# Kernel tuning notes

Hardware: AMD Instinct MI355X
Metric: run time of the kernel (lower is better)

Reference implementation:

```python
import jax, jax.numpy as jnp
import numpy as np

N_HEADS = 12
LN_EPS = 1e-5


def _layernorm(x, w):
    # torch F.layer_norm (no affine) then * w
    x = x.astype(jnp.float32)
    mu = jnp.mean(x, axis=-1, keepdims=True)
    var = jnp.mean(jnp.square(x - mu), axis=-1, keepdims=True)
    return (x - mu) * jax.lax.rsqrt(var + LN_EPS) * w


def _rotate_half(x):
    x1, x2 = jnp.split(x, 2, axis=-1)
    return jnp.concatenate([-x2, x1], axis=-1)


def setup_inputs() -> dict:
    key = jax.random.key(0)
    ks = jax.random.split(key, 10)
    b, s, dim, cond, hd = 2, 4096, 768, 768, 64
    mlp = 4 * dim
    # rotary tables
    inv_freq = 1.0 / (10000.0 ** (np.arange(0, hd, 2, dtype=np.float32) / hd))
    t = np.arange(s, dtype=np.float32)
    freqs = np.einsum('s,d->sd', t, inv_freq)           # [s, hd/2]
    emb = np.concatenate([freqs, freqs], axis=-1)        # [s, hd]
    cos = jnp.asarray(np.cos(emb))[None, :, None, None, :]
    sin = jnp.asarray(np.sin(emb))[None, :, None, None, :]
    sc = lambda f: 1.0 / np.sqrt(f)
    return {
        'x': jax.random.normal(ks[0], (b, s, dim), jnp.float32),
        'cos': cos,
        'sin': sin,
        'c': jax.random.normal(ks[1], (b, cond), jnp.float32),
        'attention_mask': jax.random.randint(ks[2], (b, s), 0, 2, jnp.int32),
        'ln1_w': jnp.ones((dim,), jnp.float32),
        'Wqkv': jax.random.normal(ks[3], (3 * dim, dim), jnp.float32) * sc(dim),
        'Wout': jax.random.normal(ks[4], (dim, dim), jnp.float32) * sc(dim),
        'ln2_w': jnp.ones((dim,), jnp.float32),
        'W1': jax.random.normal(ks[5], (mlp, dim), jnp.float32) * sc(dim),
        'b1': jnp.zeros((mlp,), jnp.float32),
        'W2': jax.random.normal(ks[6], (dim, mlp), jnp.float32) * sc(mlp),
        'b2': jnp.zeros((dim,), jnp.float32),
        'Wada': jax.random.normal(ks[7], (6 * dim, cond), jnp.float32) * 0.02,
        'bada': jnp.zeros((6 * dim,), jnp.float32),
    }


def reference(x, cos, sin, c, attention_mask, ln1_w, Wqkv, Wout, ln2_w, W1, b1, W2, b2, Wada, bada):
    b, s, dim = x.shape
    h, hd = N_HEADS, dim // N_HEADS
    # adaLN modulation: [b, 6*dim] -> six [b, 1, dim] chunks
    mod = (c @ Wada.T + bada)[:, None, :]
    shift_msa, scale_msa, gate_msa, shift_mlp, scale_mlp, gate_mlp = jnp.split(mod, 6, axis=2)

    x_skip = x
    hdn = _layernorm(x, ln1_w) * (1.0 + scale_msa) + shift_msa
    qkv = (hdn @ Wqkv.T).reshape(b, s, 3, h, hd)
    qkv = qkv * cos + _rotate_half(qkv) * sin            # RoPE on q, k, and v (as in source)
    q = jnp.transpose(qkv[:, :, 0], (0, 2, 1, 3))        # [b, h, s, hd]
    k = jnp.transpose(qkv[:, :, 1], (0, 2, 1, 3))
    v = jnp.transpose(qkv[:, :, 2], (0, 2, 1, 3))

    m = attention_mask.astype(bool)
    pair = m[:, None, :, None] & m[:, None, None, :]     # [b, 1, s, s]
    bias = jnp.where(pair, 0.0, -1e9).astype(q.dtype)

    scores = jnp.einsum('bhqd,bhkd->bhqk', q, k) / jnp.sqrt(jnp.asarray(hd, q.dtype))
    attn = jax.nn.softmax(scores + bias, axis=-1)
    o = jnp.einsum('bhqk,bhkd->bhqd', attn, v)
    o = jnp.transpose(o, (0, 2, 1, 3)).reshape(b, s, dim)

    # inference-mode bias_dropout_add_scale (dropout off)
    x = x_skip + gate_msa * (o @ Wout.T)
    h2 = _layernorm(x, ln2_w) * (1.0 + scale_mlp) + shift_mlp
    mlp = jax.nn.gelu(h2 @ W1.T + b1, approximate=True) @ W2.T + b2
    return x + gate_mlp * mlp
```

## Files before the change

### kernel.cpp

```cpp
#include <hip/hip_runtime.h>
#include <stdint.h>


typedef unsigned short u16;
typedef __attribute__((ext_vector_type(4))) float f32x4;
typedef __attribute__((ext_vector_type(8))) short short8;
typedef __attribute__((ext_vector_type(4))) short s16x4;
typedef __attribute__((ext_vector_type(8))) __bf16 bf16x8;

__device__ __forceinline__ float b2f(u16 u){
  union { unsigned int i; float f; } v; v.i = ((unsigned int)u) << 16; return v.f;
}
__device__ __forceinline__ u16 f2b(float f){
  union { float f; unsigned int i; } v; v.f = f;
  unsigned int u = v.i;
  u = u + 0x7FFFu + ((u >> 16) & 1u);
  return (u16)(u >> 16);
}
__device__ __forceinline__ f32x4 mfma16(short8 a, short8 b, f32x4 c){
  return __builtin_amdgcn_mfma_f32_16x16x32_bf16(
      __builtin_bit_cast(bf16x8, a), __builtin_bit_cast(bf16x8, b), c, 0, 0, 0);
}
__device__ __forceinline__ void gload16(const void* g, void* l){
  void* gnc = const_cast<void*>(g);
  __builtin_amdgcn_global_load_lds((__attribute__((address_space(1))) void*)gnc,
                                   (__attribute__((address_space(3))) void*)l, 16, 0, 0);
}

__global__ __launch_bounds__(256) void cvt4_k(
    const float* __restrict__ s0, u16* __restrict__ d0,
    const float* __restrict__ s1, u16* __restrict__ d1,
    const float* __restrict__ s2, u16* __restrict__ d2,
    const float* __restrict__ s3, u16* __restrict__ d3)
{
  int i = blockIdx.x*256 + threadIdx.x;
  const float* src; u16* dst; int j = i;
  if (j < 442368){ src = s0; dst = d0; }
  else if ((j -= 442368) < 147456){ src = s1; dst = d1; }
  else if ((j -= 147456) < 589824){ src = s2; dst = d2; }
  else { j -= 589824; src = s3; dst = d3; }
  float4 v = *(const float4*)(src + (size_t)j*4);
  s16x4 o; o[0]=(short)f2b(v.x); o[1]=(short)f2b(v.y);
  o[2]=(short)f2b(v.z); o[3]=(short)f2b(v.w);
  *(s16x4*)(dst + (size_t)j*4) = o;
}

__global__ __launch_bounds__(256) void kbias_k(const int* __restrict__ mask,
                                               float* __restrict__ kb,
                                               float* __restrict__ vm, int n)
{
  int i = blockIdx.x*256 + threadIdx.x;
  if (i < n) kb[i] = mask[i] ? -32.f : -1e30f;
  if (i < 24*64) vm[i] = 0.f;
}

__global__ __launch_bounds__(256) void mod_k(const float* __restrict__ c,
    const float* __restrict__ Wada, const float* __restrict__ bada, float* __restrict__ modb)
{
  int o = blockIdx.x*4 + (threadIdx.x >> 6);
  int l = threadIdx.x & 63;
  int b = o / 4608, j = o - b*4608;
  const float* cp = c + b*768;
  const float* wp = Wada + (size_t)j*768;
  float s = 0.f;
  for (int k = l; k < 768; k += 64) s += cp[k] * wp[k];
  #pragma unroll
  for (int d=1; d<64; d<<=1) s += __shfl_xor(s, d);
  if (l == 0) modb[o] = s + bada[j];
}

__global__ __launch_bounds__(256) void ln_mod_k(const float* __restrict__ xin,
    u16* __restrict__ out, const float* __restrict__ lnw, const float* __restrict__ modb,
    int shift_c, int scale_c)
{
  int row = blockIdx.x;
  int b = row >> 12;
  const float* xp = xin + (size_t)row*768;
  int t = threadIdx.x;
  float v[3]; float s = 0.f, s2 = 0.f;
  #pragma unroll
  for (int i=0;i<3;i++){ float f = xp[t + i*256]; v[i] = f; s += f; s2 += f*f; }
  #pragma unroll
  for (int d=1; d<64; d<<=1){ s += __shfl_xor(s, d); s2 += __shfl_xor(s2, d); }
  __shared__ float rs_[4], rs2_[4];
  int w = t >> 6;
  if ((t & 63) == 0){ rs_[w] = s; rs2_[w] = s2; }
  __syncthreads();
  s  = rs_[0]+rs_[1]+rs_[2]+rs_[3];
  s2 = rs2_[0]+rs2_[1]+rs2_[2]+rs2_[3];
  float mu  = s * (1.f/768.f);
  float var = fmaxf(s2 * (1.f/768.f) - mu*mu, 0.f);
  float rstd = rsqrtf(var + 1e-5f);
  const float* scp = modb + b*4608 + scale_c*768;
  const float* shp = modb + b*4608 + shift_c*768;
  #pragma unroll
  for (int i=0;i<3;i++){
    int d = t + i*256;
    float f = (v[i]-mu)*rstd*lnw[d];
    f = f*(1.f + scp[d]) + shp[d];
    out[(size_t)row*768 + d] = f2b(f);
  }
}

template<int EPI>
__global__ __launch_bounds__(256) void gemm_k(
    const u16* __restrict__ A, const u16* __restrict__ Bt, void* __restrict__ Cv,
    int M, int N, int K,
    const float* __restrict__ addend, const float* __restrict__ modb,
    const float* __restrict__ bias,
    const float* __restrict__ cosb, const float* __restrict__ sinb,
    u16* __restrict__ qO, u16* __restrict__ kO, u16* __restrict__ vO)
{
  __shared__ __align__(16) u16 As[128*64];
  __shared__ __align__(16) u16 Bs[128*64];
  const int bm = blockIdx.x, bn = blockIdx.y;
  const int tid = threadIdx.x;
  const int w = tid >> 6, l = tid & 63;
  const int wr = w >> 1, wc = w & 1;
  const int l15 = l & 15, lg = l >> 4;
  f32x4 acc[4][4] = {};

  for (int k0 = 0; k0 < K; k0 += 64){
    #pragma unroll
    for (int i=0;i<4;i++){
      int e = i*256 + tid;
      int r = e >> 3, ch = e & 7;
      int sc = ch ^ (r & 7);
      gload16(A  + (size_t)(bm*128 + r)*K + k0 + sc*8, &As[e*8]);
      gload16(Bt + (size_t)(bn*128 + r)*K + k0 + sc*8, &Bs[e*8]);
    }
    __syncthreads();
    #pragma unroll
    for (int kk=0;kk<2;kk++){
      short8 af[4], bfv[4];
      #pragma unroll
      for (int i=0;i<4;i++){
        int ra = wr*64 + i*16 + l15;
        af[i]  = *(const short8*)&As[ra*64 + (((kk*4)+lg) ^ (ra&7))*8];
        int rb = wc*64 + i*16 + l15;
        bfv[i] = *(const short8*)&Bs[rb*64 + (((kk*4)+lg) ^ (rb&7))*8];
      }
      #pragma unroll
      for (int m=0;m<4;m++)
        #pragma unroll
        for (int n=0;n<4;n++)
          acc[m][n] = mfma16(af[m], bfv[n], acc[m][n]);
    }
    __syncthreads();
  }

  if constexpr (EPI == 4){
    const int colseg = bn*128 + wc*64;
    const int qi = colseg / 768;
    const int h  = (colseg - qi*768) >> 6;
    const float qs = (qi == 0) ? 0.1803368801111601f : 1.f;
    u16* dst = (qi == 0) ? qO : (qi == 1) ? kO : vO;
    #pragma unroll
    for (int m=0;m<4;m++){
      #pragma unroll
      for (int r=0;r<4;r++){
        int row = bm*128 + wr*64 + m*16 + lg*4 + r;
        int s = row & 4095, bb = row >> 12;
        size_t obase = ((size_t)(bb*12 + h)*4096 + s)*64;
        #pragma unroll
        for (int n2=0;n2<2;n2++){
          int d1 = n2*16 + l15;
          int d2 = d1 + 32;
          float c1 = cosb[s*64 + d1], s1 = sinb[s*64 + d1];
          float c2 = cosb[s*64 + d2], s2 = sinb[s*64 + d2];
          float x1 = acc[m][n2][r], x2 = acc[m][n2+2][r];
          dst[obase + d1] = f2b((x1*c1 - x2*s1)*qs);
          dst[obase + d2] = f2b((x2*c2 + x1*s2)*qs);
        }
      }
    }
    return;
  }

  #pragma unroll
  for (int m=0;m<4;m++){
    int row0 = bm*128 + wr*64 + m*16 + lg*4;
    #pragma unroll
    for (int n=0;n<4;n++){
      int col = bn*128 + wc*64 + n*16 + l15;
      #pragma unroll
      for (int r=0;r<4;r++){
        int row = row0 + r;
        size_t idx = (size_t)row*N + col;
        float v = acc[m][n][r];
        if constexpr (EPI == 0){
          ((u16*)Cv)[idx] = f2b(v);
        } else if constexpr (EPI == 1){
          float g = modb[(row>>12)*4608 + 2*768 + col];
          ((float*)Cv)[idx] = addend[idx] + g*v;
        } else if constexpr (EPI == 2){
          float u = v + bias[col];
          float t0 = 0.7978845608028654f*(u + 0.044715f*u*u*u);
          ((u16*)Cv)[idx] = f2b(0.5f*u*(1.0f + tanhf(t0)));
        } else if constexpr (EPI == 3){
          float g = modb[(row>>12)*4608 + 5*768 + col];
          float u = v + bias[col];
          ((float*)Cv)[idx] = addend[idx] + g*u;
        }
      }
    }
  }
}

__global__ __launch_bounds__(256) void vtr_k(const u16* __restrict__ vS,
                                             u16* __restrict__ vT,
                                             float* __restrict__ vm)
{
  __shared__ __align__(16) u16 tile[64][72];
  __shared__ float cs[4][64];
  int st = blockIdx.x, bh = blockIdx.y;
  int t = threadIdx.x;
  #pragma unroll
  for (int i=0;i<2;i++){
    int e = i*256 + t;
    int r = e >> 3, d0 = (e & 7)*8;
    short8 vv = *(const short8*)(vS + ((size_t)bh*4096 + st*64 + r)*64 + d0);
    *(short8*)&tile[r][d0] = vv;
  }
  __syncthreads();
  #pragma unroll
  for (int i=0;i<2;i++){
    int e = i*256 + t;
    int d = e >> 3, s0 = (e & 7)*8;
    short8 ov;
    #pragma unroll
    for (int k2=0;k2<8;k2++) ov[k2] = (short)tile[s0+k2][d];
    *(short8*)(vT + ((size_t)bh*64 + d)*4096 + st*64 + s0) = ov;
  }
  int d = t & 63, qq = t >> 6;
  float s = 0.f;
  #pragma unroll
  for (int i=0;i<16;i++) s += b2f(tile[qq*16 + i][d]);
  cs[qq][d] = s;
  __syncthreads();
  if (qq == 0) atomicAdd(&vm[bh*64 + d], cs[0][d]+cs[1][d]+cs[2][d]+cs[3][d]);
}

#define AT_BODY(KT, KQK, KST, VPV, VST, STC, STN)                              \
{                                                                              \
  f32x4 kb_[4];                                                                \
  _Pragma("unroll")                                                            \
  for (int n=0;n<4;n++)                                                        \
    kb_[n] = *(const f32x4*)(kbrow + (KT)*64 + n*16 + lg*4);                   \
  __builtin_amdgcn_sched_barrier(0);       \
  { int k3 = (KT)+3 < 64 ? (KT)+3 : 63;                                        \
    gload16(kbase + (size_t)(k3*64+sr)*64 + ssc*8, &Ks[KST][tid*8]); }         \
  { int v2 = (KT)+2 < 64 ? (KT)+2 : 63;                                        \
    gload16(vbase + (size_t)sr*4096 + v2*64 + ssc*8, &Vs[VST][tid*8]); }       \
  if ((KT)+1 < 64){                                                            \
    __builtin_amdgcn_s_setprio(1);                                             \
    _Pragma("unroll")                                                          \
    for (int n=0;n<4;n++){                                                     \
      int R = n*16 + l15;                                                      \
      f32x4 a_ = {};                                                           \
      _Pragma("unroll")                                                        \
      for (int kk=0;kk<2;kk++){                                                \
        short8 ka = *(const short8*)&Ks[KQK][R*64 + (((kk<<2)+lg) ^ (R&7))*8]; \
        a_ = mfma16(ka, bq[kk], a_);                                           \
      }                                                                        \
      STN[n] = a_;                                                             \
    }                                                                          \
    __builtin_amdgcn_s_setprio(0);                                             \
  }                                                                            \
              \
  float p_[4][4]; float ts_ = 0.f;                                             \
  _Pragma("unroll")                                                            \
  for (int n=0;n<4;n++)                                                        \
    _Pragma("unroll")                                                          \
    for (int r=0;r<4;r++){                                                     \
      float e_ = __builtin_amdgcn_exp2f(STC[n][r] + kb_[n][r]);                \
      p_[n][r] = e_; ts_ += e_;                                                \
    }                                                                          \
  ts_ += __shfl_xor(ts_, 16);                                                  \
  ts_ += __shfl_xor(ts_, 32);                                                  \
  l_run += ts_;                                                                \
  _Pragma("unroll")                                                            \
  for (int n=0;n<4;n++){                                                       \
    unsigned p01_, p23_;                                                       \
    asm("v_cvt_pk_bf16_f32 %0, %1, %2" : "=v"(p01_) : "v"(p_[n][0]), "v"(p_[n][1])); \
    asm("v_cvt_pk_bf16_f32 %0, %1, %2" : "=v"(p23_) : "v"(p_[n][2]), "v"(p_[n][3])); \
    int s0_ = n*16 + lg*4;                                                     \
    int off_ = (((s0_>>3) ^ (l15&7))<<3) + (s0_&7);                            \
    *(unsigned*)&Ps[w][l15*64 + off_]     = p01_;                              \
    *(unsigned*)&Ps[w][l15*64 + off_ + 2] = p23_;                              \
  }                                                                            \
  __builtin_amdgcn_s_setprio(1);                                               \
  _Pragma("unroll")                                                            \
  for (int kk=0;kk<2;kk++){                                                    \
    int ch_ = (kk<<2) + lg;                                                    \
    short8 bp_ = *(const short8*)&Ps[w][l15*64 + ((ch_ ^ (l15&7))<<3)];        \
    _Pragma("unroll")                                                          \
    for (int n=0;n<4;n++){                                                     \
      int R = n*16 + l15;                                                      \
      short8 va_ = *(const short8*)&Vs[VPV][R*64 + ((ch_ ^ (R&7))<<3)];        \
      oacc[n] = mfma16(va_, bp_, oacc[n]);                                     \
    }                                                                          \
  }                                                                            \
  __builtin_amdgcn_s_setprio(0);                                               \
  __builtin_amdgcn_s_barrier();                                                \
}

__global__ __launch_bounds__(512, 4) void attn_k(
    const u16* __restrict__ qT, const u16* __restrict__ kT, const u16* __restrict__ vT,
    const int* __restrict__ mask, const float* __restrict__ kbias,
    const float* __restrict__ vmean, u16* __restrict__ o)
{
  __shared__ __align__(16) u16 Ks[4][64*64];
  __shared__ __align__(16) u16 Vs[4][64*64];
  __shared__ __align__(16) u16 Ps[8][16*64];
  const int qt = blockIdx.x, bh = blockIdx.y;
  const int b = bh / 12, h = bh - b*12;
  const int tid = threadIdx.x, w = tid >> 6, l = tid & 63;
  const int l15 = l & 15, lg = l >> 4;

  short8 bq[2];
  {
    const u16* qp = qT + ((size_t)bh*4096 + qt*128 + w*16 + l15)*64 + lg*8;
    bq[0] = *(const short8*)qp;
    bq[1] = *(const short8*)(qp + 32);
  }
  const bool fq = mask[b*4096 + qt*128 + w*16 + l15] != 0;
  const float* kbrow = kbias + b*4096;
  const u16* kbase = kT + (size_t)bh*4096*64;
  const u16* vbase = vT + (size_t)bh*64*4096;

  float l_run = 0.f;
  f32x4 oacc[4] = {};

  const int sr = tid >> 3, ssc = (tid & 7) ^ (sr & 7);

  gload16(kbase + (size_t)sr*64 + ssc*8,            &Ks[0][tid*8]);
  gload16(kbase + (size_t)(64+sr)*64 + ssc*8,       &Ks[1][tid*8]);
  gload16(kbase + (size_t)(128+sr)*64 + ssc*8,      &Ks[2][tid*8]);
  gload16(vbase + (size_t)sr*4096 + ssc*8,          &Vs[0][tid*8]);
  gload16(vbase + (size_t)sr*4096 + 64 + ssc*8,     &Vs[1][tid*8]);
  asm volatile("s_waitcnt vmcnt(0)" ::: "memory");
  __builtin_amdgcn_s_barrier();

  f32x4 stA[4], stB[4];
  #pragma unroll
  for (int n=0;n<4;n++){
    int R = n*16 + l15;
    f32x4 a_ = {};
    #pragma unroll
    for (int kk=0;kk<2;kk++){
      short8 ka = *(const short8*)&Ks[0][R*64 + (((kk<<2)+lg) ^ (R&7))*8];
      a_ = mfma16(ka, bq[kk], a_);
    }
    stA[n] = a_;
  }

  for (int kt = 0; kt < 64; kt += 4){
    AT_BODY(kt+0, 1, 3, 0, 2, stA, stB)
    AT_BODY(kt+1, 2, 0, 1, 3, stB, stA)
    AT_BODY(kt+2, 3, 1, 2, 0, stA, stB)
    AT_BODY(kt+3, 0, 2, 3, 1, stB, stA)
  }

  float inv = 1.f / l_run;
  size_t base = ((size_t)b*4096 + qt*128 + w*16 + l15)*768 + h*64 + lg*4;
  #pragma unroll
  for (int n=0;n<4;n++){
    f32x4 vm = *(const f32x4*)(vmean + bh*64 + n*16 + lg*4);
    float v0 = fq ? oacc[n][0]*inv : vm[0]*(1.f/4096.f);
    float v1 = fq ? oacc[n][1]*inv : vm[1]*(1.f/4096.f);
    float v2 = fq ? oacc[n][2]*inv : vm[2]*(1.f/4096.f);
    float v3 = fq ? oacc[n][3]*inv : vm[3]*(1.f/4096.f);
    unsigned q01 = (unsigned)f2b(v0) | ((unsigned)f2b(v1) << 16);
    unsigned q23 = (unsigned)f2b(v2) | ((unsigned)f2b(v3) << 16);
    *(unsigned*)&o[base + n*16]     = q01;
    *(unsigned*)&o[base + n*16 + 2] = q23;
  }
}

extern "C" void kernel_launch(void* const* d_in, const int* in_sizes, int n_in,
                              void* d_out, int out_size, void* d_ws, size_t ws_size,
                              hipStream_t stream)
{
  const float* x    = (const float*)d_in[0];
  const float* cosb = (const float*)d_in[1];
  const float* sinb = (const float*)d_in[2];
  const float* c    = (const float*)d_in[3];
  const int* amask  = (const int*)d_in[4];
  const float* ln1w = (const float*)d_in[5];
  const float* Wqkv = (const float*)d_in[6];
  const float* Wout = (const float*)d_in[7];
  const float* ln2w = (const float*)d_in[8];
  const float* W1   = (const float*)d_in[9];
  const float* b1   = (const float*)d_in[10];
  const float* W2   = (const float*)d_in[11];
  const float* b2   = (const float*)d_in[12];
  const float* Wada = (const float*)d_in[13];
  const float* bada = (const float*)d_in[14];

  char* ws = (char*)d_ws;
  size_t off = 0;
  auto take = [&](size_t bytes)->char*{
    char* p = ws + off; off = (off + bytes + 255) & ~(size_t)255; return p;
  };
  float* modb = (float*)take(9216*sizeof(float));
  float* kbias= (float*)take(8192*sizeof(float));
  float* vmean= (float*)take(24*64*sizeof(float));
  u16* hdn  = (u16*)take((size_t)8192*768*2);
  u16* bufA = (u16*)take((size_t)8192*3072*2);
  u16* vS   = (u16*)take((size_t)8192*768*2);
  u16* qTb  = (u16*)take((size_t)8192*768*2);
  u16* kTb  = (u16*)take((size_t)8192*768*2);
  u16* vTb  = (u16*)take((size_t)8192*768*2);
  u16* ob   = (u16*)take((size_t)8192*768*2);
  u16* WqkvB= (u16*)take((size_t)2304*768*2);
  u16* WoutB= (u16*)take((size_t)768*768*2);
  u16* W1B  = (u16*)take((size_t)3072*768*2);
  u16* W2B  = (u16*)take((size_t)768*3072*2);
  float* out = (float*)d_out;
  float* x1 = out;

  cvt4_k<<<6912, 256, 0, stream>>>(Wqkv, WqkvB, Wout, WoutB, W1, W1B, W2, W2B);
  kbias_k<<<32, 256, 0, stream>>>(amask, kbias, vmean, 8192);

  mod_k  <<<2304, 256, 0, stream>>>(c, Wada, bada, modb);
  ln_mod_k<<<8192, 256, 0, stream>>>(x, hdn, ln1w, modb, 0, 1);
  gemm_k<4><<<dim3(64,18), 256, 0, stream>>>(hdn, WqkvB, nullptr, 8192, 2304, 768,
                                             nullptr, nullptr, nullptr,
                                             cosb, sinb, qTb, kTb, vS);
  vtr_k  <<<dim3(64,24), 256, 0, stream>>>(vS, vTb, vmean);
  attn_k <<<dim3(32,24), 512, 0, stream>>>(qTb, kTb, vTb, amask, kbias, vmean, ob);
  gemm_k<1><<<dim3(64,6), 256, 0, stream>>>(ob, WoutB, x1, 8192, 768, 768,
                                            x, modb, nullptr,
                                            nullptr, nullptr, nullptr, nullptr, nullptr);
  ln_mod_k<<<8192, 256, 0, stream>>>(x1, hdn, ln2w, modb, 3, 4);
  gemm_k<2><<<dim3(64,24), 256, 0, stream>>>(hdn, W1B, bufA, 8192, 3072, 768,
                                             nullptr, nullptr, b1,
                                             nullptr, nullptr, nullptr, nullptr, nullptr);
  gemm_k<3><<<dim3(64,6), 256, 0, stream>>>(bufA, W2B, out, 8192, 768, 3072,
                                            x1, modb, b2,
                                            nullptr, nullptr, nullptr, nullptr, nullptr);
}
```

Baseline: 396.0 us.

## Split attention over two KV halves and combine partials in a new kernel

The attention kernel now splits the 4096-key range into two halves along a third grid dimension. Each block writes unnormalized fp32 partial outputs and row sums to scratch space that reuses the bufA and hdn workspace. A new combine kernel adds the partials, normalizes, applies the masked-query fallback to the V mean, and writes bf16. This doubles the block count from 768 to 1536 so the GPU fills better, at the cost of roughly 50MB of extra fp32 traffic and an additional launch. It relies on no running-max rescaling (a fixed softmax shift), so partials combine by plain addition. The launch-bounds occupancy hint is also dropped.

Result: no change. 396.6 us (+0.2%).

```diff
diff --git a/kernel.cpp b/kernel.cpp
--- a/kernel.cpp
+++ b/kernel.cpp
@@ -248,11 +248,11 @@
   for (int n=0;n<4;n++)                                                        \
     kb_[n] = *(const f32x4*)(kbrow + (KT)*64 + n*16 + lg*4);                   \
   __builtin_amdgcn_sched_barrier(0);       \
-  { int k3 = (KT)+3 < 64 ? (KT)+3 : 63;                                        \
+  { int k3 = (KT)+3 < kend ? (KT)+3 : kend-1;                                  \
     gload16(kbase + (size_t)(k3*64+sr)*64 + ssc*8, &Ks[KST][tid*8]); }         \
-  { int v2 = (KT)+2 < 64 ? (KT)+2 : 63;                                        \
+  { int v2 = (KT)+2 < kend ? (KT)+2 : kend-1;                                  \
     gload16(vbase + (size_t)sr*4096 + v2*64 + ssc*8, &Vs[VST][tid*8]); }       \
-  if ((KT)+1 < 64){                                                            \
+  if ((KT)+1 < kend){                                                          \
     __builtin_amdgcn_s_setprio(1);                                             \
     _Pragma("unroll")                                                          \
     for (int n=0;n<4;n++){                                                     \
@@ -305,18 +305,18 @@
   __builtin_amdgcn_s_barrier();                                                \
 }
 
-__global__ __launch_bounds__(512, 4) void attn_k(
+__global__ __launch_bounds__(512) void attn_k(
     const u16* __restrict__ qT, const u16* __restrict__ kT, const u16* __restrict__ vT,
-    const int* __restrict__ mask, const float* __restrict__ kbias,
-    const float* __restrict__ vmean, u16* __restrict__ o)
+    const float* __restrict__ kbias, float* __restrict__ po, float* __restrict__ pl)
 {
   __shared__ __align__(16) u16 Ks[4][64*64];
   __shared__ __align__(16) u16 Vs[4][64*64];
   __shared__ __align__(16) u16 Ps[8][16*64];
-  const int qt = blockIdx.x, bh = blockIdx.y;
-  const int b = bh / 12, h = bh - b*12;
+  const int qt = blockIdx.x, bh = blockIdx.y, kv = blockIdx.z;
+  const int b = bh / 12;
   const int tid = threadIdx.x, w = tid >> 6, l = tid & 63;
   const int l15 = l & 15, lg = l >> 4;
+  const int k0 = kv*32, kend = k0 + 32;
 
   short8 bq[2];
   {
@@ -324,10 +324,9 @@
     bq[0] = *(const short8*)qp;
     bq[1] = *(const short8*)(qp + 32);
   }
-  const bool fq = mask[b*4096 + qt*128 + w*16 + l15] != 0;
-  const float* kbrow = kbias + b*4096;
-  const u16* kbase = kT + (size_t)bh*4096*64;
-  const u16* vbase = vT + (size_t)bh*64*4096;
+  const float* kbrow = kbias + b*4096 + k0*64;
+  const u16* kbase = kT + (size_t)bh*4096*64 + (size_t)k0*64*64;
+  const u16* vbase = vT + (size_t)bh*64*4096 + (size_t)k0*64;
 
   float l_run = 0.f;
   f32x4 oacc[4] = {};
@@ -355,26 +354,39 @@
     stA[n] = a_;
   }
 
-  for (int kt = 0; kt < 64; kt += 4){
+  for (int kt = 0; kt < 32; kt += 4){
     AT_BODY(kt+0, 1, 3, 0, 2, stA, stB)
     AT_BODY(kt+1, 2, 0, 1, 3, stB, stA)
     AT_BODY(kt+2, 3, 1, 2, 0, stA, stB)
     AT_BODY(kt+3, 0, 2, 3, 1, stB, stA)
   }
 
-  float inv = 1.f / l_run;
-  size_t base = ((size_t)b*4096 + qt*128 + w*16 + l15)*768 + h*64 + lg*4;
-  #pragma unroll
-  for (int n=0;n<4;n++){
-    f32x4 vm = *(const f32x4*)(vmean + bh*64 + n*16 + lg*4);
-    float v0 = fq ? oacc[n][0]*inv : vm[0]*(1.f/4096.f);
-    float v1 = fq ? oacc[n][1]*inv : vm[1]*(1.f/4096.f);
-    float v2 = fq ? oacc[n][2]*inv : vm[2]*(1.f/4096.f);
-    float v3 = fq ? oacc[n][3]*inv : vm[3]*(1.f/4096.f);
-    unsigned q01 = (unsigned)f2b(v0) | ((unsigned)f2b(v1) << 16);
-    unsigned q23 = (unsigned)f2b(v2) | ((unsigned)f2b(v3) << 16);
-    *(unsigned*)&o[base + n*16]     = q01;
-    *(unsigned*)&o[base + n*16 + 2] = q23;
+  const int qrow = qt*128 + w*16 + l15;
+  float* pob = po + (((size_t)kv*24 + bh)*4096 + qrow)*64;
+  #pragma unroll
+  for (int n=0;n<4;n++)
+    *(f32x4*)&pob[n*16 + lg*4] = oacc[n];
+  if (lg == 0) pl[((size_t)kv*24 + bh)*4096 + qrow] = l_run;
+}
+
+__global__ __launch_bounds__(256) void comb_k(const float* __restrict__ po,
+    const float* __restrict__ pl, const int* __restrict__ mask,
+    const float* __restrict__ vm, u16* __restrict__ o)
+{
+  int row = blockIdx.x;
+  int b = row >> 12, s = row & 4095;
+  bool fq = mask[row] != 0;
+  int t = threadIdx.x;
+  #pragma unroll
+  for (int i=0;i<3;i++){
+    int j = t + i*256;
+    int h = j >> 6, d = j & 63;
+    size_t pi = (((size_t)b*12 + h)*4096 + s)*64 + d;
+    size_t li = ((size_t)b*12 + h)*4096 + s;
+    float O = po[pi] + po[(size_t)24*4096*64 + pi];
+    float L = pl[li] + pl[(size_t)24*4096 + li];
+    float v = fq ? O / L : vm[(b*12 + h)*64 + d]*(1.f/4096.f);
+    o[(size_t)row*768 + j] = f2b(v);
   }
 }
 
@@ -419,6 +431,8 @@
   u16* W2B  = (u16*)take((size_t)768*3072*2);
   float* out = (float*)d_out;
   float* x1 = out;
+  float* po = (float*)bufA;
+  float* pl = (float*)hdn;
 
   cvt4_k<<<6912, 256, 0, stream>>>(Wqkv, WqkvB, Wout, WoutB, W1, W1B, W2, W2B);
   kbias_k<<<32, 256, 0, stream>>>(amask, kbias, vmean, 8192);
@@ -429,7 +443,8 @@
                                              nullptr, nullptr, nullptr,
                                              cosb, sinb, qTb, kTb, vS);
   vtr_k  <<<dim3(64,24), 256, 0, stream>>>(vS, vTb, vmean);
-  attn_k <<<dim3(32,24), 512, 0, stream>>>(qTb, kTb, vTb, amask, kbias, vmean, ob);
+  attn_k <<<dim3(32,24,2), 512, 0, stream>>>(qTb, kTb, vTb, kbias, po, pl);
+  comb_k <<<8192, 256, 0, stream>>>(po, pl, amask, vmean, ob);
   gemm_k<1><<<dim3(64,6), 256, 0, stream>>>(ob, WoutB, x1, 8192, 768, 768,
                                             x, modb, nullptr,
                                             nullptr, nullptr, nullptr, nullptr, nullptr);
```
